# Optimization experiments

Hardware: AMD Instinct MI355X
Metric: run time of the kernel (lower is better)

Reference implementation:

```python
import jax, jax.numpy as jnp
import numpy as np

B, S, D_MODEL, N_HEADS = 2, 2048, 2048, 16
HEAD_DIM = D_MODEL // N_HEADS
SCALE = 1.0 / np.sqrt(HEAD_DIM)
SOFTCAP = 30.0
NEG = -10000.0


def _apply_rope(h):
    # h: [B, S, H, D]; faithful to torch ref: repeat_interleave'd cos/sin with
    # half-split rotate_half.
    seq, d = h.shape[1], h.shape[3]
    pos = jnp.arange(seq, dtype=jnp.float32)
    inv_freq = 1.0 / (10000.0 ** (jnp.arange(0, d, 2, dtype=jnp.float32) / d))
    phase = pos[:, None] * inv_freq[None, :]                      # [S, D/2]
    cos = jnp.repeat(jnp.cos(phase), 2, axis=-1)[None, :, None, :].astype(h.dtype)
    sin = jnp.repeat(jnp.sin(phase), 2, axis=-1)[None, :, None, :].astype(h.dtype)
    rot = jnp.concatenate([-h[..., d // 2:], h[..., :d // 2]], axis=-1)
    return h * cos + rot * sin


def setup_inputs() -> dict:
    key = jax.random.key(0)
    k1, k2, k3, k4, k5 = jax.random.split(key, 5)
    hidden_states = jax.random.normal(k1, (B, S, D_MODEL), dtype=jnp.float32)
    # causal allowed-attention mask [S, S]; True = attention permitted
    allowed_attention = jnp.tril(jnp.ones((S, S), dtype=bool))
    # no padding (True would mean padded position)
    padding_mask = jnp.zeros((B, S), dtype=bool)
    std = 1.0 / np.sqrt(D_MODEL)
    Wq = jax.random.normal(k2, (D_MODEL, D_MODEL), dtype=jnp.float32) * std
    Wk = jax.random.normal(k3, (D_MODEL, D_MODEL), dtype=jnp.float32) * std
    Wv = jax.random.normal(k4, (D_MODEL, D_MODEL), dtype=jnp.float32) * std
    Wo = jax.random.normal(k5, (D_MODEL, D_MODEL), dtype=jnp.float32) * std
    return {"hidden_states": hidden_states, "allowed_attention": allowed_attention,
            "padding_mask": padding_mask, "Wq": Wq, "Wk": Wk, "Wv": Wv, "Wo": Wo}


def reference(hidden_states, allowed_attention, padding_mask, Wq, Wk, Wv, Wo):
    b, s, _ = hidden_states.shape
    q = (hidden_states @ Wq.T).reshape(b, s, N_HEADS, HEAD_DIM)
    k = (hidden_states @ Wk.T).reshape(b, s, N_HEADS, HEAD_DIM)
    v = (hidden_states @ Wv.T).reshape(b, s, N_HEADS, HEAD_DIM)
    q = _apply_rope(q)
    k = _apply_rope(k)
    logits = jnp.einsum('bthd,bshd->bhts', q, k).astype(jnp.float32) * SCALE
    logits = SOFTCAP * jnp.tanh(logits / SOFTCAP)
    logits = jnp.where(allowed_attention[None, None, :, :], logits, NEG)
    logits = jnp.where(padding_mask[:, None, None, :], NEG, logits)
    weights = jax.nn.softmax(logits, axis=-1).astype(q.dtype)
    attended = jnp.einsum('bhts,bshd->bthd', weights, v).reshape(b, s, D_MODEL)
    out = attended @ Wo.T
    return jnp.where(padding_mask[:, :, None], 0.0, out)
```

## Files before the change

kernel.cpp:

```cpp
#include <hip/hip_runtime.h>
#include <hip/hip_bf16.h>

#define S_LEN 2048
#define NH    16
#define HD    128
#define BHN   32
#define DM    2048
#define MTOK  4096
#define NT_QKV 32

typedef __attribute__((ext_vector_type(8))) short short8;
typedef __attribute__((ext_vector_type(4))) float f32x4;

__device__ __forceinline__ unsigned short f2bf(float x){
  union { __hip_bfloat16 h; unsigned short u; } c; c.h = __float2bfloat16(x); return c.u;
}
__device__ __forceinline__ float bf2f(unsigned short u){
  union { unsigned short u; __hip_bfloat16 h; } c; c.u = u; return __bfloat162float(c.h);
}

__global__ void cvt_kernel(const float* __restrict__ src, unsigned short* __restrict__ dst, int n4){
  int i = blockIdx.x*256 + threadIdx.x;
  if (i >= n4) return;
  float4 v = reinterpret_cast<const float4*>(src)[i];
  ushort4 o;
  o.x = f2bf(v.x); o.y = f2bf(v.y); o.z = f2bf(v.z); o.w = f2bf(v.w);
  reinterpret_cast<ushort4*>(dst)[i] = o;
}

__global__ void cvt_w_kernel(const float* __restrict__ s0, const float* __restrict__ s1,
                             const float* __restrict__ s2, const float* __restrict__ s3,
                             unsigned short* __restrict__ dqkv, unsigned short* __restrict__ dwo,
                             int n4each){
  int which = blockIdx.y;
  const float* src = (which==0) ? s0 : (which==1) ? s1 : (which==2) ? s2 : s3;
  unsigned short* dst = (which<3) ? (dqkv + (size_t)which*DM*DM) : dwo;
  int i = blockIdx.x*256 + threadIdx.x;
  if (i >= n4each) return;
  float4 v = reinterpret_cast<const float4*>(src)[i];
  ushort4 o;
  o.x = f2bf(v.x); o.y = f2bf(v.y); o.z = f2bf(v.z); o.w = f2bf(v.w);
  reinterpret_cast<ushort4*>(dst)[i] = o;
}

__global__ void rope_table_kernel(float* __restrict__ cosT, float* __restrict__ sinT){
  int s = blockIdx.x, i = threadIdx.x;
  float inv = powf(10000.f, -(float)i * (1.f/64.f));
  float ph = (float)s * inv;
  float sv, cv; sincosf(ph, &sv, &cv);
  cosT[s*64 + i] = cv; sinT[s*64 + i] = sv;
}

__global__ void rope_apply2_kernel(unsigned short* __restrict__ Q, unsigned short* __restrict__ K,
                                   const float* __restrict__ cosT, const float* __restrict__ sinT){
  int gid = blockIdx.x*256 + threadIdx.x;
  unsigned short* X = (gid < (BHN*S_LEN*64)) ? Q : K;
  int g = gid & (BHN*S_LEN*64 - 1);
  int j = g & 63, row = g >> 6, s = row & (S_LEN-1);
  unsigned short* p = X + (size_t)row*HD;
  float h0 = bf2f(p[j]), h1 = bf2f(p[j+64]);
  int f0 = j >> 1;
  float c0 = cosT[s*64+f0],    s0 = sinT[s*64+f0];
  float c1 = cosT[s*64+32+f0], s1 = sinT[s*64+32+f0];
  p[j]    = f2bf(h0*c0 - h1*s0);
  p[j+64] = f2bf(h1*c1 + h0*s1);
}

#define MFMA_Q(ACC) \
  __builtin_amdgcn_s_setprio(1); \
  _Pragma("unroll") \
  for (int mi=0;mi<4;++mi){ \
    _Pragma("unroll") \
    for (int nj=0;nj<2;++nj){ \
      ACC[mi][nj] = __builtin_amdgcn_mfma_f32_16x16x32_bf16(af[mi*2+0], bf[nj*2+0], ACC[mi][nj], 0,0,0); \
      ACC[mi][nj] = __builtin_amdgcn_mfma_f32_16x16x32_bf16(af[mi*2+1], bf[nj*2+1], ACC[mi][nj], 0,0,0); \
    } \
  } \
  __builtin_amdgcn_s_setprio(0);

__global__ __launch_bounds__(512, 2)
void gemm_qkv_256(const unsigned short* __restrict__ A, const unsigned short* __restrict__ B,
                  unsigned short* __restrict__ Cq, unsigned short* __restrict__ Ck,
                  unsigned short* __restrict__ Cv){
  extern __shared__ unsigned char sm[];
  const int t = threadIdx.x;
  const int lane = t & 63, w = t >> 6;
  const int lr = lane & 15, lg = lane >> 4;
  const int wm = w >> 2, wn = w & 3;
  int id = blockIdx.x;
  int swz = (id & 7)*48 + (id >> 3);
  const int bm = swz / 24, bn = swz % 24;
  const size_t rs = (size_t)DM*2;
  const unsigned char* Ab = (const unsigned char*)A + (size_t)bm*256*rs;
  const unsigned char* Bb = (const unsigned char*)B + (size_t)bn*256*rs;
  const int r0 = t >> 3, c0 = t & 7;

  auto stage = [&](int tkt, int slot){
    if (tkt >= NT_QKV) return;
    const unsigned char* ob = (slot < 2) ? Ab : Bb;
    const unsigned char* sb = ob + (size_t)((slot & 1) ? 128 : 0)*rs + (size_t)tkt*128;
    unsigned char* hb = sm + ((tkt & 1) ? 65536 : 0) + slot*16384;
    __builtin_amdgcn_global_load_lds(
        (const unsigned int*)(sb + (size_t)r0*rs + ((unsigned)(c0 ^ (r0 & 7)) << 4)),
        (unsigned int*)(hb + t*16), 16, 0, 0);
    int r1 = r0 + 64;
    __builtin_amdgcn_global_load_lds(
        (const unsigned int*)(sb + (size_t)r1*rs + ((unsigned)(c0 ^ (r1 & 7)) << 4)),
        (unsigned int*)(hb + 8192 + t*16), 16, 0, 0);
  };

  const int xr = lr & 7;
  const int cK0 = ((0 + lg) ^ xr) << 4;
  const int cK1 = ((4 + lg) ^ xr) << 4;

  short8 af[8], bf[4];
  auto loadA = [&](int d, int rh){
    const unsigned char* hb = sm + d*65536 + rh*16384;
#pragma unroll
    for (int mi=0;mi<4;++mi){
      int rb = (wm*64 + mi*16 + lr)*128;
      af[mi*2+0] = *reinterpret_cast<const short8*>(hb + rb + cK0);
      af[mi*2+1] = *reinterpret_cast<const short8*>(hb + rb + cK1);
    }
  };
  auto loadB = [&](int d, int ch){
    const unsigned char* hb = sm + d*65536 + (2+ch)*16384;
#pragma unroll
    for (int nj=0;nj<2;++nj){
      int rb = (wn*32 + nj*16 + lr)*128;
      bf[nj*2+0] = *reinterpret_cast<const short8*>(hb + rb + cK0);
      bf[nj*2+1] = *reinterpret_cast<const short8*>(hb + rb + cK1);
    }
  };

  f32x4 acc00[4][2] = {}, acc01[4][2] = {}, acc11[4][2] = {}, acc10[4][2] = {};

  stage(0,0); stage(0,2); stage(0,3); stage(0,1);
  stage(1,0); stage(1,3); stage(1,1);
  asm volatile("s_waitcnt vmcnt(6)" ::: "memory");
  __builtin_amdgcn_s_barrier();

  for (int g = 0; g < NT_QKV; ++g){
    const int d = g & 1;
    loadA(d, 0); loadB(d, 0);
    stage(g+1, 2);
    __builtin_amdgcn_s_barrier();
    MFMA_Q(acc00);
    __builtin_amdgcn_s_barrier();
    loadB(d, 1);
    stage(g+2, 0);
    __builtin_amdgcn_s_barrier();
    MFMA_Q(acc01);
    __builtin_amdgcn_s_barrier();
    loadA(d, 1);
    stage(g+2, 3);
    __builtin_amdgcn_s_barrier();
    MFMA_Q(acc11);
    __builtin_amdgcn_s_barrier();
    loadB(d, 0);
    stage(g+2, 1);
    __builtin_amdgcn_s_barrier();
    MFMA_Q(acc10);
    if (g < NT_QKV-1){
      if (g == NT_QKV-2) { asm volatile("s_waitcnt vmcnt(0)" ::: "memory"); }
      else               { asm volatile("s_waitcnt vmcnt(6)" ::: "memory"); }
    }
    __builtin_amdgcn_s_barrier();
  }

  auto epi = [&](const f32x4 (*acc)[2], int rh, int ch){
#pragma unroll
    for (int mi=0;mi<4;++mi)
#pragma unroll
    for (int nj=0;nj<2;++nj){
      int col  = bn*256 + ch*128 + wn*32 + nj*16 + lr;
      int rowb = bm*256 + rh*128 + wm*64 + mi*16 + lg*4;
      if (col < 4096){
        unsigned short* dst = (col < 2048) ? Cq : Ck;
        int cc = col & 2047, h = cc >> 7, dd = cc & 127;
#pragma unroll
        for (int rr=0;rr<4;++rr){
          int row = rowb + rr, bb = row >> 11, s = row & 2047;
          dst[(((size_t)(bb*16+h)*2048 + s)<<7) + dd] = f2bf(acc[mi][nj][rr]);
        }
      } else {
        int cc = col - 4096, h = cc >> 7, dd = cc & 127;
        ushort4 pk;
        pk.x = f2bf(acc[mi][nj][0]); pk.y = f2bf(acc[mi][nj][1]);
        pk.z = f2bf(acc[mi][nj][2]); pk.w = f2bf(acc[mi][nj][3]);
        int bb = rowb >> 11, s = rowb & 2047, kb = s >> 6, kvl = s & 63;
        *reinterpret_cast<ushort4*>(&Cv[(((size_t)((bb*16+h)*32 + kb)*128 + dd)<<6) + kvl]) = pk;
      }
    }
  };
  epi(acc00,0,0); epi(acc01,0,1); epi(acc11,1,1); epi(acc10,1,0);
}

__global__ __launch_bounds__(256)
void gemm_wo(const unsigned short* __restrict__ A, const unsigned short* __restrict__ B,
             float* __restrict__ C, int M, int N, int K){
  __shared__ __align__(16) unsigned char As[2][8192];
  __shared__ __align__(16) unsigned char Bs[2][8192];
  const int t = threadIdx.x;
  const int lane = t & 63, w = t >> 6;
  const int lr = lane & 15, lg = lane >> 4;
  const int wr = (w >> 1)*64, wc = (w & 1)*64;
  const int bm = blockIdx.y, bn = blockIdx.x;
  const int rowstride = K*2;
  const int nk = rowstride >> 6;
  const unsigned char* Ab = (const unsigned char*)A + (size_t)bm*128*rowstride;
  const unsigned char* Bb = (const unsigned char*)B + (size_t)bn*128*rowstride;
  unsigned int L0 = (unsigned int)(w*2+0)*1024u + (unsigned int)lane*16u;
  unsigned int L1 = (unsigned int)(w*2+1)*1024u + (unsigned int)lane*16u;
  const unsigned char* aS0 = Ab + (size_t)(L0>>6)*rowstride + (L0&63u);
  const unsigned char* aS1 = Ab + (size_t)(L1>>6)*rowstride + (L1&63u);
  const unsigned char* bS0 = Bb + (size_t)(L0>>6)*rowstride + (L0&63u);
  const unsigned char* bS1 = Bb + (size_t)(L1>>6)*rowstride + (L1&63u);
  f32x4 acc[4][4] = {};
  __builtin_amdgcn_global_load_lds((const unsigned int*)(aS0), (unsigned int*)(&As[0][L0]), 16,0,0);
  __builtin_amdgcn_global_load_lds((const unsigned int*)(bS0), (unsigned int*)(&Bs[0][L0]), 16,0,0);
  __builtin_amdgcn_global_load_lds((const unsigned int*)(aS1), (unsigned int*)(&As[0][L1]), 16,0,0);
  __builtin_amdgcn_global_load_lds((const unsigned int*)(bS1), (unsigned int*)(&Bs[0][L1]), 16,0,0);
  __syncthreads();
  int cur = 0;
  for (int kt = 0; kt < nk; ++kt){
    if (kt + 1 < nk){
      int ktb = (kt+1) << 6;
      __builtin_amdgcn_global_load_lds((const unsigned int*)(aS0 + ktb), (unsigned int*)(&As[cur^1][L0]), 16,0,0);
      __builtin_amdgcn_global_load_lds((const unsigned int*)(bS0 + ktb), (unsigned int*)(&Bs[cur^1][L0]), 16,0,0);
      __builtin_amdgcn_global_load_lds((const unsigned int*)(aS1 + ktb), (unsigned int*)(&As[cur^1][L1]), 16,0,0);
      __builtin_amdgcn_global_load_lds((const unsigned int*)(bS1 + ktb), (unsigned int*)(&Bs[cur^1][L1]), 16,0,0);
    }
    short8 af[4], bfr[4];
#pragma unroll
    for (int mi=0;mi<4;++mi)
      af[mi]  = *reinterpret_cast<const short8*>(&As[cur][(size_t)(wr+mi*16+lr)*64 + lg*16]);
#pragma unroll
    for (int nj=0;nj<4;++nj)
      bfr[nj] = *reinterpret_cast<const short8*>(&Bs[cur][(size_t)(wc+nj*16+lr)*64 + lg*16]);
    __builtin_amdgcn_s_setprio(1);
#pragma unroll
    for (int mi=0;mi<4;++mi)
#pragma unroll
      for (int nj=0;nj<4;++nj)
        acc[mi][nj] = __builtin_amdgcn_mfma_f32_16x16x32_bf16(af[mi], bfr[nj], acc[mi][nj], 0,0,0);
    __builtin_amdgcn_s_setprio(0);
    __syncthreads();
    cur ^= 1;
  }
#pragma unroll
  for (int mi=0;mi<4;++mi)
#pragma unroll
    for (int nj=0;nj<4;++nj)
#pragma unroll
      for (int r=0;r<4;++r){
        int row = bm*128 + wr + mi*16 + lg*4 + r;
        int col = bn*128 + wc + nj*16 + lr;
        C[(size_t)row*N + col] = acc[mi][nj][r];
      }
}

__global__ __launch_bounds__(256, 2)
void attn_kernel(const unsigned short* __restrict__ Qr, const unsigned short* __restrict__ Kr,
                 const unsigned short* __restrict__ Vp, unsigned short* __restrict__ AO){
  const int bid = blockIdx.x;
  const int qb  = 15 - (bid >> 5);
  const int bh  = bid & 31;
  const int t = threadIdx.x;
  const int w = t >> 6, lane = t & 63, lr = lane & 15, lg = lane >> 4;
  const int qbase = qb*128 + w*32;
  const int diag_w = (qbase + 31) >> 6;
  const int kmax = qb*2 + 1;
  const unsigned short* Qh = Qr + (size_t)bh*S_LEN*HD;
  const unsigned char*  Kg = (const unsigned char*)(Kr + (size_t)bh*S_LEN*HD);
  const unsigned char*  Vg = (const unsigned char*)Vp + (size_t)bh*32*16384;

  __shared__ __align__(16) unsigned short Ks[8192];
  __shared__ __align__(16) unsigned short Vs[8192];
  __shared__ __align__(16) unsigned short Ps[4][32][72];

  short8 qa[2][4];
#pragma unroll
  for (int f=0;f<2;++f)
#pragma unroll
    for (int kc=0;kc<4;++kc)
      qa[f][kc] = *reinterpret_cast<const short8*>(&Qh[(size_t)(qbase + f*16 + lr)*HD + kc*32 + lg*8]);

  float lsum[2] = {0.f, 0.f};
  f32x4 o[2][8] = {};

  const float C1 = 2.f * 0.08838834764831845f * 1.4426950408889634f / 30.f;
  const float C2 = -60.f * 1.4426950408889634f;

  for (int kb = 0; kb <= kmax; ++kb){
    const unsigned char* Kt = Kg + (size_t)kb*(64*256);
    const unsigned char* Vt = Vg + (size_t)kb*16384;
#pragma unroll
    for (int j=0;j<4;++j){
      unsigned int L  = (unsigned int)(w*4+j)*1024u + (unsigned int)lane*16u;
      unsigned int rK = L >> 8;
      unsigned int sK = (L & 255u) ^ ((rK & 15u) << 4);
      __builtin_amdgcn_global_load_lds((const unsigned int*)(Kt + (rK<<8) + sK),
          (unsigned int*)((unsigned char*)Ks + (size_t)(w*4+j)*1024), 16, 0, 0);
      unsigned int rV = L >> 7;
      unsigned int sV = (L & 127u) ^ ((rV & 7u) << 4);
      __builtin_amdgcn_global_load_lds((const unsigned int*)(Vt + (rV<<7) + sV),
          (unsigned int*)((unsigned char*)Vs + (size_t)(w*4+j)*1024), 16, 0, 0);
    }
    __syncthreads();
    if (kb <= diag_w){
      f32x4 s[2][4] = {};
      __builtin_amdgcn_s_setprio(1);
#pragma unroll
      for (int nf=0;nf<4;++nf)
#pragma unroll
        for (int kc=0;kc<4;++kc){
          unsigned int byt = ((unsigned int)(nf*16+lr) << 8) + (((unsigned int)(kc*64 + lg*16)) ^ ((unsigned int)(lr&15) << 4));
          short8 kf = *reinterpret_cast<const short8*>((const unsigned char*)Ks + byt);
          s[0][nf] = __builtin_amdgcn_mfma_f32_16x16x32_bf16(kf, qa[0][kc], s[0][nf], 0,0,0);
          s[1][nf] = __builtin_amdgcn_mfma_f32_16x16x32_bf16(kf, qa[1][kc], s[1][nf], 0,0,0);
        }
      __builtin_amdgcn_s_setprio(0);
#pragma unroll
      for (int f=0;f<2;++f){
#pragma unroll
        for (int nf=0;nf<4;++nf){
#pragma unroll
          for (int r=0;r<4;++r){
            float u = __builtin_amdgcn_exp2f(s[f][nf][r] * C1);
            float p = __builtin_amdgcn_exp2f(C2 * __builtin_amdgcn_rcpf(u + 1.f));
            if (kb == diag_w){
              int kvi = kb*64 + nf*16 + lg*4 + r;
              if (kvi > qbase + f*16 + lr) p = 0.f;
            }
            s[f][nf][r] = p;
            lsum[f] += p;
          }
          ushort4 pk;
          pk.x = f2bf(s[f][nf][0]); pk.y = f2bf(s[f][nf][1]);
          pk.z = f2bf(s[f][nf][2]); pk.w = f2bf(s[f][nf][3]);
          *reinterpret_cast<ushort4*>(&Ps[w][f*16+lr][nf*16 + lg*4]) = pk;
        }
      }
      short8 pb[2][2];
#pragma unroll
      for (int f=0;f<2;++f)
#pragma unroll
        for (int kc2=0;kc2<2;++kc2)
          pb[f][kc2] = *reinterpret_cast<const short8*>(&Ps[w][f*16+lr][kc2*32 + lg*8]);
      __builtin_amdgcn_s_setprio(1);
#pragma unroll
      for (int df=0;df<8;++df)
#pragma unroll
        for (int kc2=0;kc2<2;++kc2){
          unsigned int byt = ((unsigned int)(df*16+lr) << 7) + (((unsigned int)(kc2*64 + lg*16)) ^ ((unsigned int)(lr&7) << 4));
          short8 vb = *reinterpret_cast<const short8*>((const unsigned char*)Vs + byt);
          o[0][df] = __builtin_amdgcn_mfma_f32_16x16x32_bf16(vb, pb[0][kc2], o[0][df], 0,0,0);
          o[1][df] = __builtin_amdgcn_mfma_f32_16x16x32_bf16(vb, pb[1][kc2], o[1][df], 0,0,0);
        }
      __builtin_amdgcn_s_setprio(0);
    }
    __syncthreads();
  }
#pragma unroll
  for (int f=0;f<2;++f){
    lsum[f] += __shfl_xor(lsum[f], 16);
    lsum[f] += __shfl_xor(lsum[f], 32);
  }
  const int bb = bh >> 4, h = bh & 15;
#pragma unroll
  for (int f=0;f<2;++f){
    const float inv = 1.f / lsum[f];
    const int qi = qbase + f*16 + lr;
#pragma unroll
    for (int df=0;df<8;++df){
      ushort4 pk;
      pk.x = f2bf(o[f][df][0] * inv); pk.y = f2bf(o[f][df][1] * inv);
      pk.z = f2bf(o[f][df][2] * inv); pk.w = f2bf(o[f][df][3] * inv);
      *reinterpret_cast<ushort4*>(&AO[((size_t)(bb*S_LEN + qi))*DM + h*HD + df*16 + lg*4]) = pk;
    }
  }
}

extern "C" void kernel_launch(void* const* d_in, const int* in_sizes, int n_in,
                              void* d_out, int out_size, void* d_ws, size_t ws_size,
                              hipStream_t stream){
  const float* hs = (const float*)d_in[0];
  const float* Wq = (const float*)d_in[3];
  const float* Wk = (const float*)d_in[4];
  const float* Wv = (const float*)d_in[5];
  const float* Wo = (const float*)d_in[6];

  uint8_t* base = (uint8_t*)d_ws;
  unsigned short* hsb  = (unsigned short*)base; base += (size_t)MTOK*DM*2;
  unsigned short* wqkv = (unsigned short*)base; base += (size_t)3*DM*DM*2;
  unsigned short* wob  = (unsigned short*)base; base += (size_t)DM*DM*2;
  unsigned short* Qr   = (unsigned short*)base; base += (size_t)MTOK*DM*2;
  unsigned short* Kr   = (unsigned short*)base; base += (size_t)MTOK*DM*2;
  unsigned short* Vp   = (unsigned short*)base; base += (size_t)MTOK*DM*2;
  unsigned short* AO   = (unsigned short*)base; base += (size_t)MTOK*DM*2;
  float* cosT = (float*)base;                   base += (size_t)S_LEN*64*4;
  float* sinT = (float*)base;                   base += (size_t)S_LEN*64*4;

  cvt_kernel<<<(MTOK*DM/4)/256, 256, 0, stream>>>(hs, hsb, MTOK*DM/4);
  cvt_w_kernel<<<dim3((DM*DM/4)/256, 4), 256, 0, stream>>>(Wq, Wk, Wv, Wo, wqkv, wob, DM*DM/4);
  rope_table_kernel<<<S_LEN, 64, 0, stream>>>(cosT, sinT);

  hipFuncSetAttribute((const void*)gemm_qkv_256,
                      hipFuncAttributeMaxDynamicSharedMemorySize, 131072);
  gemm_qkv_256<<<384, 512, 131072, stream>>>(hsb, wqkv, Qr, Kr, Vp);

  rope_apply2_kernel<<<(2*BHN*S_LEN*64)/256, 256, 0, stream>>>(Qr, Kr, cosT, sinT);

  attn_kernel<<<512, 256, 0, stream>>>(Qr, Kr, Vp, AO);

  gemm_wo<<<dim3(16, 32), 256, 0, stream>>>(AO, wob, (float*)d_out, MTOK, DM, DM);
}
```

Measured before the change: 294.4 us.

## Unify QKV and output GEMMs into templated 256x128 pipelined kernel; rebalance attention order

Replaces the 256x256 QKV GEMM and the simple 128x128 double-buffered Wo GEMM with one templated 256x128-tile, 8-wave kernel that uses the same swizzled global_load_lds pipeline. The QKV launch goes from 384 to 768 blocks and the Wo launch to 256 larger blocks using 96KB of LDS. The attention block order now also pairs heavy and light causal q-blocks, so the second half of the grid runs ascending. This aims for better CU occupancy and wave balance and a better-pipelined output projection, at the cost of less operand reuse per tile.

Result: faster. 285.1 us (-3.2%).

```diff
diff --git a/kernel.cpp b/kernel.cpp
--- a/kernel.cpp
+++ b/kernel.cpp
@@ -7,7 +7,7 @@
 #define BHN   32
 #define DM    2048
 #define MTOK  4096
-#define NT_QKV 32
+#define NTK   32
 
 typedef __attribute__((ext_vector_type(8))) short short8;
 typedef __attribute__((ext_vector_type(4))) float f32x4;
@@ -66,205 +66,146 @@
   p[j+64] = f2bf(h1*c1 + h0*s1);
 }
 
-#define MFMA_Q(ACC) \
+#define MFMA8(ACC) \
   __builtin_amdgcn_s_setprio(1); \
   _Pragma("unroll") \
   for (int mi=0;mi<4;++mi){ \
-    _Pragma("unroll") \
-    for (int nj=0;nj<2;++nj){ \
-      ACC[mi][nj] = __builtin_amdgcn_mfma_f32_16x16x32_bf16(af[mi*2+0], bf[nj*2+0], ACC[mi][nj], 0,0,0); \
-      ACC[mi][nj] = __builtin_amdgcn_mfma_f32_16x16x32_bf16(af[mi*2+1], bf[nj*2+1], ACC[mi][nj], 0,0,0); \
-    } \
+    ACC[mi] = __builtin_amdgcn_mfma_f32_16x16x32_bf16(af[mi*2+0], bf[0], ACC[mi], 0,0,0); \
+    ACC[mi] = __builtin_amdgcn_mfma_f32_16x16x32_bf16(af[mi*2+1], bf[1], ACC[mi], 0,0,0); \
   } \
   __builtin_amdgcn_s_setprio(0);
 
-__global__ __launch_bounds__(512, 2)
-void gemm_qkv_256(const unsigned short* __restrict__ A, const unsigned short* __restrict__ B,
-                  unsigned short* __restrict__ Cq, unsigned short* __restrict__ Ck,
-                  unsigned short* __restrict__ Cv){
+template<int MODE>
+__global__ __launch_bounds__(512)
+void gemm_8p(const unsigned short* __restrict__ A, const unsigned short* __restrict__ B,
+             float* __restrict__ C0, unsigned short* __restrict__ Cq,
+             unsigned short* __restrict__ Ck, unsigned short* __restrict__ Cv){
   extern __shared__ unsigned char sm[];
   const int t = threadIdx.x;
   const int lane = t & 63, w = t >> 6;
   const int lr = lane & 15, lg = lane >> 4;
   const int wm = w >> 2, wn = w & 3;
-  int id = blockIdx.x;
-  int swz = (id & 7)*48 + (id >> 3);
-  const int bm = swz / 24, bn = swz % 24;
-  const size_t rs = (size_t)DM*2;
+  int id = blockIdx.x, bm, bn;
+  if (MODE == 3){ int swz = (id & 7)*96 + (id >> 3); bm = swz/48; bn = swz%48; }
+  else          { int swz = (id & 7)*32 + (id >> 3); bm = swz/16; bn = swz%16; }
+  const size_t rs = 4096;
   const unsigned char* Ab = (const unsigned char*)A + (size_t)bm*256*rs;
-  const unsigned char* Bb = (const unsigned char*)B + (size_t)bn*256*rs;
+  const unsigned char* Bb = (const unsigned char*)B + (size_t)bn*128*rs;
   const int r0 = t >> 3, c0 = t & 7;
 
   auto stage = [&](int tkt, int slot){
-    if (tkt >= NT_QKV) return;
-    const unsigned char* ob = (slot < 2) ? Ab : Bb;
-    const unsigned char* sb = ob + (size_t)((slot & 1) ? 128 : 0)*rs + (size_t)tkt*128;
-    unsigned char* hb = sm + ((tkt & 1) ? 65536 : 0) + slot*16384;
-    __builtin_amdgcn_global_load_lds(
-        (const unsigned int*)(sb + (size_t)r0*rs + ((unsigned)(c0 ^ (r0 & 7)) << 4)),
-        (unsigned int*)(hb + t*16), 16, 0, 0);
-    int r1 = r0 + 64;
-    __builtin_amdgcn_global_load_lds(
-        (const unsigned int*)(sb + (size_t)r1*rs + ((unsigned)(c0 ^ (r1 & 7)) << 4)),
-        (unsigned int*)(hb + 8192 + t*16), 16, 0, 0);
+    if (tkt >= NTK) return;
+    unsigned char* hb = sm + ((tkt & 1) ? 49152 : 0);
+    if (slot < 2){
+      const unsigned char* sb = Ab + (size_t)(slot ? 128 : 0)*rs + (size_t)tkt*128;
+      hb += slot*16384;
+      __builtin_amdgcn_global_load_lds(
+          (const unsigned int*)(sb + (size_t)r0*rs + ((unsigned)(c0 ^ (r0 & 7)) << 4)),
+          (unsigned int*)(hb + t*16), 16, 0, 0);
+      int r1 = r0 + 64;
+      __builtin_amdgcn_global_load_lds(
+          (const unsigned int*)(sb + (size_t)r1*rs + ((unsigned)(c0 ^ (r1 & 7)) << 4)),
+          (unsigned int*)(hb + 8192 + t*16), 16, 0, 0);
+    } else {
+      const unsigned char* sb = Bb + (size_t)((slot-2) ? 64 : 0)*rs + (size_t)tkt*128;
+      hb += 32768 + (slot-2)*8192;
+      __builtin_amdgcn_global_load_lds(
+          (const unsigned int*)(sb + (size_t)r0*rs + ((unsigned)(c0 ^ (r0 & 7)) << 4)),
+          (unsigned int*)(hb + t*16), 16, 0, 0);
+    }
   };
 
-  const int xr = lr & 7;
-  const int cK0 = ((0 + lg) ^ xr) << 4;
-  const int cK1 = ((4 + lg) ^ xr) << 4;
-
-  short8 af[8], bf[4];
+  short8 af[8], bf[2];
   auto loadA = [&](int d, int rh){
-    const unsigned char* hb = sm + d*65536 + rh*16384;
 #pragma unroll
     for (int mi=0;mi<4;++mi){
-      int rb = (wm*64 + mi*16 + lr)*128;
-      af[mi*2+0] = *reinterpret_cast<const short8*>(hb + rb + cK0);
-      af[mi*2+1] = *reinterpret_cast<const short8*>(hb + rb + cK1);
+      int row = wm*64 + mi*16 + lr;
+      const unsigned char* rp = sm + d*49152 + rh*16384 + row*128;
+      int x = row & 7;
+      af[mi*2+0] = *reinterpret_cast<const short8*>(rp + (((0+lg) ^ x) << 4));
+      af[mi*2+1] = *reinterpret_cast<const short8*>(rp + (((4+lg) ^ x) << 4));
     }
   };
   auto loadB = [&](int d, int ch){
-    const unsigned char* hb = sm + d*65536 + (2+ch)*16384;
-#pragma unroll
-    for (int nj=0;nj<2;++nj){
-      int rb = (wn*32 + nj*16 + lr)*128;
-      bf[nj*2+0] = *reinterpret_cast<const short8*>(hb + rb + cK0);
-      bf[nj*2+1] = *reinterpret_cast<const short8*>(hb + rb + cK1);
-    }
+    int row = wn*16 + lr;
+    const unsigned char* rp = sm + d*49152 + 32768 + ch*8192 + row*128;
+    int x = row & 7;
+    bf[0] = *reinterpret_cast<const short8*>(rp + (((0+lg) ^ x) << 4));
+    bf[1] = *reinterpret_cast<const short8*>(rp + (((4+lg) ^ x) << 4));
   };
 
-  f32x4 acc00[4][2] = {}, acc01[4][2] = {}, acc11[4][2] = {}, acc10[4][2] = {};
+  f32x4 acc00[4] = {}, acc01[4] = {}, acc11[4] = {}, acc10[4] = {};
 
   stage(0,0); stage(0,2); stage(0,3); stage(0,1);
   stage(1,0); stage(1,3); stage(1,1);
-  asm volatile("s_waitcnt vmcnt(6)" ::: "memory");
+  asm volatile("s_waitcnt vmcnt(5)" ::: "memory");
   __builtin_amdgcn_s_barrier();
 
-  for (int g = 0; g < NT_QKV; ++g){
+  for (int g = 0; g < NTK; ++g){
     const int d = g & 1;
     loadA(d, 0); loadB(d, 0);
     stage(g+1, 2);
     __builtin_amdgcn_s_barrier();
-    MFMA_Q(acc00);
+    MFMA8(acc00);
     __builtin_amdgcn_s_barrier();
     loadB(d, 1);
     stage(g+2, 0);
     __builtin_amdgcn_s_barrier();
-    MFMA_Q(acc01);
+    MFMA8(acc01);
     __builtin_amdgcn_s_barrier();
     loadA(d, 1);
     stage(g+2, 3);
     __builtin_amdgcn_s_barrier();
-    MFMA_Q(acc11);
+    MFMA8(acc11);
     __builtin_amdgcn_s_barrier();
     loadB(d, 0);
     stage(g+2, 1);
     __builtin_amdgcn_s_barrier();
-    MFMA_Q(acc10);
-    if (g < NT_QKV-1){
-      if (g == NT_QKV-2) { asm volatile("s_waitcnt vmcnt(0)" ::: "memory"); }
-      else               { asm volatile("s_waitcnt vmcnt(6)" ::: "memory"); }
+    MFMA8(acc10);
+    if (g < NTK-1){
+      if (g == NTK-2) { asm volatile("s_waitcnt vmcnt(0)" ::: "memory"); }
+      else            { asm volatile("s_waitcnt vmcnt(5)" ::: "memory"); }
     }
     __builtin_amdgcn_s_barrier();
   }
 
-  auto epi = [&](const f32x4 (*acc)[2], int rh, int ch){
-#pragma unroll
-    for (int mi=0;mi<4;++mi)
-#pragma unroll
-    for (int nj=0;nj<2;++nj){
-      int col  = bn*256 + ch*128 + wn*32 + nj*16 + lr;
+  auto epi = [&](const f32x4* acc, int rh, int ch){
+#pragma unroll
+    for (int mi=0;mi<4;++mi){
+      int col  = bn*128 + ch*64 + wn*16 + lr;
       int rowb = bm*256 + rh*128 + wm*64 + mi*16 + lg*4;
-      if (col < 4096){
-        unsigned short* dst = (col < 2048) ? Cq : Ck;
-        int cc = col & 2047, h = cc >> 7, dd = cc & 127;
-#pragma unroll
-        for (int rr=0;rr<4;++rr){
-          int row = rowb + rr, bb = row >> 11, s = row & 2047;
-          dst[(((size_t)(bb*16+h)*2048 + s)<<7) + dd] = f2bf(acc[mi][nj][rr]);
+      if (MODE == 0){
+#pragma unroll
+        for (int rr=0;rr<4;++rr)
+          C0[(size_t)(rowb+rr)*DM + col] = acc[mi][rr];
+      } else {
+        if (col < 4096){
+          unsigned short* dst = (col < 2048) ? Cq : Ck;
+          int cc = col & 2047, h = cc >> 7, dd = cc & 127;
+#pragma unroll
+          for (int rr=0;rr<4;++rr){
+            int row = rowb + rr, bb = row >> 11, s = row & 2047;
+            dst[(((size_t)(bb*16+h)*2048 + s)<<7) + dd] = f2bf(acc[mi][rr]);
+          }
+        } else {
+          int cc = col - 4096, h = cc >> 7, dd = cc & 127;
+          ushort4 pk;
+          pk.x = f2bf(acc[mi][0]); pk.y = f2bf(acc[mi][1]);
+          pk.z = f2bf(acc[mi][2]); pk.w = f2bf(acc[mi][3]);
+          int bb = rowb >> 11, s = rowb & 2047, kb = s >> 6, kvl = s & 63;
+          *reinterpret_cast<ushort4*>(&Cv[(((size_t)((bb*16+h)*32 + kb)*128 + dd)<<6) + kvl]) = pk;
         }
-      } else {
-        int cc = col - 4096, h = cc >> 7, dd = cc & 127;
-        ushort4 pk;
-        pk.x = f2bf(acc[mi][nj][0]); pk.y = f2bf(acc[mi][nj][1]);
-        pk.z = f2bf(acc[mi][nj][2]); pk.w = f2bf(acc[mi][nj][3]);
-        int bb = rowb >> 11, s = rowb & 2047, kb = s >> 6, kvl = s & 63;
-        *reinterpret_cast<ushort4*>(&Cv[(((size_t)((bb*16+h)*32 + kb)*128 + dd)<<6) + kvl]) = pk;
       }
     }
   };
   epi(acc00,0,0); epi(acc01,0,1); epi(acc11,1,1); epi(acc10,1,0);
-}
-
-__global__ __launch_bounds__(256)
-void gemm_wo(const unsigned short* __restrict__ A, const unsigned short* __restrict__ B,
-             float* __restrict__ C, int M, int N, int K){
-  __shared__ __align__(16) unsigned char As[2][8192];
-  __shared__ __align__(16) unsigned char Bs[2][8192];
-  const int t = threadIdx.x;
-  const int lane = t & 63, w = t >> 6;
-  const int lr = lane & 15, lg = lane >> 4;
-  const int wr = (w >> 1)*64, wc = (w & 1)*64;
-  const int bm = blockIdx.y, bn = blockIdx.x;
-  const int rowstride = K*2;
-  const int nk = rowstride >> 6;
-  const unsigned char* Ab = (const unsigned char*)A + (size_t)bm*128*rowstride;
-  const unsigned char* Bb = (const unsigned char*)B + (size_t)bn*128*rowstride;
-  unsigned int L0 = (unsigned int)(w*2+0)*1024u + (unsigned int)lane*16u;
-  unsigned int L1 = (unsigned int)(w*2+1)*1024u + (unsigned int)lane*16u;
-  const unsigned char* aS0 = Ab + (size_t)(L0>>6)*rowstride + (L0&63u);
-  const unsigned char* aS1 = Ab + (size_t)(L1>>6)*rowstride + (L1&63u);
-  const unsigned char* bS0 = Bb + (size_t)(L0>>6)*rowstride + (L0&63u);
-  const unsigned char* bS1 = Bb + (size_t)(L1>>6)*rowstride + (L1&63u);
-  f32x4 acc[4][4] = {};
-  __builtin_amdgcn_global_load_lds((const unsigned int*)(aS0), (unsigned int*)(&As[0][L0]), 16,0,0);
-  __builtin_amdgcn_global_load_lds((const unsigned int*)(bS0), (unsigned int*)(&Bs[0][L0]), 16,0,0);
-  __builtin_amdgcn_global_load_lds((const unsigned int*)(aS1), (unsigned int*)(&As[0][L1]), 16,0,0);
-  __builtin_amdgcn_global_load_lds((const unsigned int*)(bS1), (unsigned int*)(&Bs[0][L1]), 16,0,0);
-  __syncthreads();
-  int cur = 0;
-  for (int kt = 0; kt < nk; ++kt){
-    if (kt + 1 < nk){
-      int ktb = (kt+1) << 6;
-      __builtin_amdgcn_global_load_lds((const unsigned int*)(aS0 + ktb), (unsigned int*)(&As[cur^1][L0]), 16,0,0);
-      __builtin_amdgcn_global_load_lds((const unsigned int*)(bS0 + ktb), (unsigned int*)(&Bs[cur^1][L0]), 16,0,0);
-      __builtin_amdgcn_global_load_lds((const unsigned int*)(aS1 + ktb), (unsigned int*)(&As[cur^1][L1]), 16,0,0);
-      __builtin_amdgcn_global_load_lds((const unsigned int*)(bS1 + ktb), (unsigned int*)(&Bs[cur^1][L1]), 16,0,0);
-    }
-    short8 af[4], bfr[4];
-#pragma unroll
-    for (int mi=0;mi<4;++mi)
-      af[mi]  = *reinterpret_cast<const short8*>(&As[cur][(size_t)(wr+mi*16+lr)*64 + lg*16]);
-#pragma unroll
-    for (int nj=0;nj<4;++nj)
-      bfr[nj] = *reinterpret_cast<const short8*>(&Bs[cur][(size_t)(wc+nj*16+lr)*64 + lg*16]);
-    __builtin_amdgcn_s_setprio(1);
-#pragma unroll
-    for (int mi=0;mi<4;++mi)
-#pragma unroll
-      for (int nj=0;nj<4;++nj)
-        acc[mi][nj] = __builtin_amdgcn_mfma_f32_16x16x32_bf16(af[mi], bfr[nj], acc[mi][nj], 0,0,0);
-    __builtin_amdgcn_s_setprio(0);
-    __syncthreads();
-    cur ^= 1;
-  }
-#pragma unroll
-  for (int mi=0;mi<4;++mi)
-#pragma unroll
-    for (int nj=0;nj<4;++nj)
-#pragma unroll
-      for (int r=0;r<4;++r){
-        int row = bm*128 + wr + mi*16 + lg*4 + r;
-        int col = bn*128 + wc + nj*16 + lr;
-        C[(size_t)row*N + col] = acc[mi][nj][r];
-      }
 }
 
 __global__ __launch_bounds__(256, 2)
 void attn_kernel(const unsigned short* __restrict__ Qr, const unsigned short* __restrict__ Kr,
                  const unsigned short* __restrict__ Vp, unsigned short* __restrict__ AO){
   const int bid = blockIdx.x;
-  const int qb  = 15 - (bid >> 5);
+  const int qb  = (bid < 256) ? (15 - (bid >> 5)) : ((bid >> 5) - 8);
   const int bh  = bid & 31;
   const int t = threadIdx.x;
   const int w = t >> 6, lane = t & 63, lr = lane & 15, lg = lane >> 4;
@@ -406,13 +347,16 @@
   cvt_w_kernel<<<dim3((DM*DM/4)/256, 4), 256, 0, stream>>>(Wq, Wk, Wv, Wo, wqkv, wob, DM*DM/4);
   rope_table_kernel<<<S_LEN, 64, 0, stream>>>(cosT, sinT);
 
-  hipFuncSetAttribute((const void*)gemm_qkv_256,
-                      hipFuncAttributeMaxDynamicSharedMemorySize, 131072);
-  gemm_qkv_256<<<384, 512, 131072, stream>>>(hsb, wqkv, Qr, Kr, Vp);
+  hipFuncSetAttribute((const void*)gemm_8p<3>,
+                      hipFuncAttributeMaxDynamicSharedMemorySize, 98304);
+  hipFuncSetAttribute((const void*)gemm_8p<0>,
+                      hipFuncAttributeMaxDynamicSharedMemorySize, 98304);
+
+  gemm_8p<3><<<768, 512, 98304, stream>>>(hsb, wqkv, nullptr, Qr, Kr, Vp);
 
   rope_apply2_kernel<<<(2*BHN*S_LEN*64)/256, 256, 0, stream>>>(Qr, Kr, cosT, sinT);
 
   attn_kernel<<<512, 256, 0, stream>>>(Qr, Kr, Vp, AO);
 
-  gemm_wo<<<dim3(16, 32), 256, 0, stream>>>(AO, wob, (float*)d_out, MTOK, DM, DM);
-}
+  gemm_8p<0><<<256, 512, 98304, stream>>>(AO, wob, (float*)d_out, nullptr, nullptr, nullptr);
+}
```
